# Kernel optimization log

Measured on AMD Instinct MI355X. Metric: run time of the kernel, lower is better.

Reference implementation:

```python
import jax, jax.numpy as jnp
import numpy as np

N_NODES = 200000
N_EDGES = 400000
NUM_GRAPHS = 8192
NODE_DIM, EDGE_DIM, H, NCLS, NLAYERS = 80, 6, 128, 500, 4


def setup_inputs() -> dict:
    key = jax.random.key(0)
    ks = iter(jax.random.split(key, 32))
    s = 0.05
    inp = {
        "x": jax.random.normal(next(ks), (N_NODES, NODE_DIM), jnp.float32),
        "edge_index": jax.random.randint(next(ks), (2, N_EDGES), 0, N_NODES, jnp.int32),
        "edge_attr": jax.random.uniform(next(ks), (N_EDGES, EDGE_DIM), jnp.float32),
        # sorted segment ids covering all NUM_GRAPHS graphs (~24 nodes each)
        "batch": ((jnp.arange(N_NODES, dtype=jnp.int64) * NUM_GRAPHS) // N_NODES).astype(jnp.int32),
        "node_w": jax.random.normal(next(ks), (NODE_DIM, H), jnp.float32) * s,
        "node_b": jnp.zeros((H,), jnp.float32),
        "edge_w": jax.random.normal(next(ks), (EDGE_DIM, H), jnp.float32) * s,
        "edge_b": jnp.zeros((H,), jnp.float32),
        "conv_w1": jax.random.normal(next(ks), (NLAYERS, H, 2 * H), jnp.float32) * s,
        "conv_b1": jnp.zeros((NLAYERS, 2 * H), jnp.float32),
        "conv_bn1_g": jnp.ones((NLAYERS, 2 * H), jnp.float32),
        "conv_bn1_b": jnp.zeros((NLAYERS, 2 * H), jnp.float32),
        "conv_w2": jax.random.normal(next(ks), (NLAYERS, 2 * H, H), jnp.float32) * s,
        "conv_b2": jnp.zeros((NLAYERS, H), jnp.float32),
        "bn_g": jnp.ones((NLAYERS, H), jnp.float32),
        "bn_b": jnp.zeros((NLAYERS, H), jnp.float32),
        "cls_w1": jax.random.normal(next(ks), (2 * H, H), jnp.float32) * s,
        "cls_b1": jnp.zeros((H,), jnp.float32),
        "cls_bn_g": jnp.ones((H,), jnp.float32),
        "cls_bn_b": jnp.zeros((H,), jnp.float32),
        "cls_w2": jax.random.normal(next(ks), (H, NCLS), jnp.float32) * s,
        "cls_b2": jnp.zeros((NCLS,), jnp.float32),
    }
    return inp


def _bn(h, g, b, eps=1e-5):
    # training-mode BatchNorm1d: biased batch statistics over dim 0
    m = h.mean(0)
    v = h.var(0)
    return (h - m) * jax.lax.rsqrt(v + eps) * g + b


def reference(x, edge_index, edge_attr, batch,
              node_w, node_b, edge_w, edge_b,
              conv_w1, conv_b1, conv_bn1_g, conv_bn1_b,
              conv_w2, conv_b2, bn_g, bn_b,
              cls_w1, cls_b1, cls_bn_g, cls_bn_b, cls_w2, cls_b2):
    n = x.shape[0]
    h = x @ node_w + node_b                       # [N, H]
    ea = edge_attr @ edge_w + edge_b              # [E, H]
    src, dst = edge_index[0], edge_index[1]       # PyG: row=source j, col=target i
    for l in range(conv_w1.shape[0]):
        # GINEConv: nn((1+eps)*x + sum_j relu(x_j + e_ij)), eps=0
        msg = jax.nn.relu(h[src] + ea)            # [E, H] gather + add + relu
        agg = jax.ops.segment_sum(msg, dst, num_segments=n)
        z = h + agg
        z = jax.nn.relu(_bn(z @ conv_w1[l] + conv_b1[l], conv_bn1_g[l], conv_bn1_b[l]))
        h = z @ conv_w2[l] + conv_b2[l]
        h = jax.nn.relu(_bn(h, bn_g[l], bn_b[l]))
    # global mean + max pooling over graphs
    counts = jax.ops.segment_sum(jnp.ones((n, 1), h.dtype), batch, num_segments=NUM_GRAPHS)
    pmean = jax.ops.segment_sum(h, batch, num_segments=NUM_GRAPHS) / jnp.maximum(counts, 1.0)
    pmax = jax.ops.segment_max(h, batch, num_segments=NUM_GRAPHS)
    pmax = jnp.where(jnp.isfinite(pmax), pmax, 0.0)
    p = jnp.concatenate([pmean, pmax], axis=1)    # [G, 2H]
    z = jax.nn.relu(p @ cls_w1 + cls_b1)
    z = _bn(z, cls_bn_g, cls_bn_b)                # dropout: identity (eval)
    return z @ cls_w2 + cls_b2                    # [G, NCLS]
```

## Files before the change

### kernel.cpp

```cpp
#include <hip/hip_runtime.h>

#define NN 200000
#define NE 400000
#define NG 8192
#define HD 128
#define H2 256
#define ND 80
#define NC 500
#define ZBLK 240
#define NCHUNK 6250

typedef short bf16x8 __attribute__((ext_vector_type(8)));
typedef short bf16x4 __attribute__((ext_vector_type(4)));
typedef float f32x4  __attribute__((ext_vector_type(4)));

static __device__ __forceinline__ short f2bf(float f) {
    unsigned u = __float_as_uint(f);
    unsigned r = (u + 0x7fffu + ((u >> 16) & 1u)) >> 16;
    return (short)r;
}
static __device__ __forceinline__ float bf2f(short s) {
    return __uint_as_float(((unsigned)(unsigned short)s) << 16);
}

__global__ void k_zero(float* p, int n) {
    int i = blockIdx.x * 256 + threadIdx.x;
    if (i < n) p[i] = 0.f;
}

__global__ __launch_bounds__(256) void k_node_encode(
    const float* __restrict__ x, const float* __restrict__ w,
    const float* __restrict__ b, float* __restrict__ u, float* __restrict__ agg)
{
    __shared__ float ws[ND][HD];
    __shared__ float xs[32][ND];
    const int tid = threadIdx.x;
    for (int i = tid; i < ND * HD; i += 256) ws[i >> 7][i & 127] = w[i];
    const int row0 = blockIdx.x * 32;
    for (int i = tid; i < 32 * ND; i += 256) {
        int r = i / ND, c = i % ND;
        xs[r][c] = x[(size_t)(row0 + r) * ND + c];
    }
    __syncthreads();
    const int col = tid & 127, rs = tid >> 7;
    const float bias = b[col];
    for (int it = 0; it < 16; ++it) {
        int rl = it * 2 + rs;
        float acc = bias;
        #pragma unroll
        for (int k = 0; k < ND; ++k) acc += xs[rl][k] * ws[k][col];
        size_t gi = (size_t)(row0 + rl) * HD + col;
        u[gi] = acc;
        agg[gi] = 0.f;
    }
}

__global__ __launch_bounds__(256) void k_msg_agg(
    const float* __restrict__ u, const int* __restrict__ ei,
    const float* __restrict__ eattr, const float* __restrict__ ew,
    const float* __restrict__ eb, const float* __restrict__ s2,
    const float* __restrict__ sh2, float* __restrict__ agg, int first)
{
    __shared__ float ews[6][HD];
    __shared__ float ebs[HD], s2s[HD], sh2s[HD];
    const int tid = threadIdx.x;
    for (int i = tid; i < 6 * HD; i += 256) ews[i >> 7][i & 127] = ew[i];
    if (tid < HD) { ebs[tid] = eb[tid]; s2s[tid] = s2[tid]; sh2s[tid] = sh2[tid]; }
    __syncthreads();
    const int col = tid & 127, es = tid >> 7;
    const int e0 = blockIdx.x * 32;
    for (int it = 0; it < 16; ++it) {
        int e = e0 + it * 2 + es;
        int src = ei[e], dst = ei[NE + e];
        float a0 = eattr[e * 6 + 0], a1 = eattr[e * 6 + 1], a2 = eattr[e * 6 + 2];
        float a3 = eattr[e * 6 + 3], a4 = eattr[e * 6 + 4], a5 = eattr[e * 6 + 5];
        float hv = u[(size_t)src * HD + col];
        if (!first) hv = fmaxf(hv * s2s[col] + sh2s[col], 0.f);
        float m = hv + ebs[col]
                + a0 * ews[0][col] + a1 * ews[1][col] + a2 * ews[2][col]
                + a3 * ews[3][col] + a4 * ews[4][col] + a5 * ews[5][col];
        m = fmaxf(m, 0.f);
        atomicAdd(&agg[(size_t)dst * HD + col], m);
    }
}

__global__ __launch_bounds__(256) void k_zstats2(
    const float* __restrict__ u, const float* __restrict__ agg,
    const float* __restrict__ s2, const float* __restrict__ sh2,
    float* __restrict__ Mpart, float* __restrict__ colzPart, int first)
{
    __shared__ float zs[32][HD];
    __shared__ float cred[8][HD];
    const int tid = threadIdx.x;
    const int bid = blockIdx.x;
    const int i0 = (tid >> 5) * 16;
    const int j0 = (tid & 31) * 4;
    const int lrow = tid >> 5;
    const int lc4  = tid & 31;

    float4 sv = *(const float4*)(s2 + lc4 * 4);
    float4 shv = *(const float4*)(sh2 + lc4 * 4);

    float acc[16][4];
    #pragma unroll
    for (int a = 0; a < 16; ++a)
        #pragma unroll
        for (int b = 0; b < 4; ++b) acc[a][b] = 0.f;
    float4 csum = make_float4(0.f, 0.f, 0.f, 0.f);

    float4 pv[4];
    int chunk = bid;
    {
        const size_t r0 = (size_t)chunk * 32;
        #pragma unroll
        for (int i = 0; i < 4; ++i) {
            size_t gi = (r0 + lrow + i * 8) * HD + lc4 * 4;
            float4 hv = *(const float4*)(u + gi);
            float4 av = *(const float4*)(agg + gi);
            if (!first) {
                hv.x = fmaxf(hv.x * sv.x + shv.x, 0.f);
                hv.y = fmaxf(hv.y * sv.y + shv.y, 0.f);
                hv.z = fmaxf(hv.z * sv.z + shv.z, 0.f);
                hv.w = fmaxf(hv.w * sv.w + shv.w, 0.f);
            }
            pv[i] = make_float4(hv.x + av.x, hv.y + av.y, hv.z + av.z, hv.w + av.w);
        }
    }

    while (chunk < NCHUNK) {
        __syncthreads();
        #pragma unroll
        for (int i = 0; i < 4; ++i) {
            *(float4*)(&zs[lrow + i * 8][lc4 * 4]) = pv[i];
            csum.x += pv[i].x; csum.y += pv[i].y;
            csum.z += pv[i].z; csum.w += pv[i].w;
        }
        __syncthreads();
        int nxt = chunk + ZBLK;
        if (nxt < NCHUNK) {
            const size_t r0 = (size_t)nxt * 32;
            #pragma unroll
            for (int i = 0; i < 4; ++i) {
                size_t gi = (r0 + lrow + i * 8) * HD + lc4 * 4;
                float4 hv = *(const float4*)(u + gi);
                float4 av = *(const float4*)(agg + gi);
                if (!first) {
                    hv.x = fmaxf(hv.x * sv.x + shv.x, 0.f);
                    hv.y = fmaxf(hv.y * sv.y + shv.y, 0.f);
                    hv.z = fmaxf(hv.z * sv.z + shv.z, 0.f);
                    hv.w = fmaxf(hv.w * sv.w + shv.w, 0.f);
                }
                pv[i] = make_float4(hv.x + av.x, hv.y + av.y, hv.z + av.z, hv.w + av.w);
            }
        }
        #pragma unroll 8
        for (int r = 0; r < 32; ++r) {
            float4 zj  = *(const float4*)(&zs[r][j0]);
            float4 zi0 = *(const float4*)(&zs[r][i0]);
            float4 zi1 = *(const float4*)(&zs[r][i0 + 4]);
            float4 zi2 = *(const float4*)(&zs[r][i0 + 8]);
            float4 zi3 = *(const float4*)(&zs[r][i0 + 12]);
            float zi[16] = {zi0.x, zi0.y, zi0.z, zi0.w,
                            zi1.x, zi1.y, zi1.z, zi1.w,
                            zi2.x, zi2.y, zi2.z, zi2.w,
                            zi3.x, zi3.y, zi3.z, zi3.w};
            #pragma unroll
            for (int a = 0; a < 16; ++a) {
                acc[a][0] += zi[a] * zj.x;
                acc[a][1] += zi[a] * zj.y;
                acc[a][2] += zi[a] * zj.z;
                acc[a][3] += zi[a] * zj.w;
            }
        }
        chunk = nxt;
    }

    float* mp = Mpart + (size_t)bid * 16384;
    #pragma unroll
    for (int a = 0; a < 16; ++a)
        *(float4*)(mp + (i0 + a) * HD + j0) =
            make_float4(acc[a][0], acc[a][1], acc[a][2], acc[a][3]);

    *(float4*)(&cred[lrow][lc4 * 4]) = csum;
    __syncthreads();
    if (tid < HD) {
        float s = 0.f;
        #pragma unroll
        for (int k = 0; k < 8; ++k) s += cred[k][tid];
        colzPart[bid * HD + tid] = s;
    }
}

__global__ __launch_bounds__(256) void k_mreduce(
    const float* __restrict__ Mpart, const float* __restrict__ colzPart,
    float* __restrict__ M, float* __restrict__ colz)
{
    int idx = blockIdx.x * 256 + threadIdx.x;
    if (idx < 16384) {
        float s = 0.f;
        for (int b = 0; b < ZBLK; ++b) s += Mpart[(size_t)b * 16384 + idx];
        M[idx] = s;
    } else if (idx < 16384 + HD) {
        int c = idx - 16384;
        float s = 0.f;
        for (int b = 0; b < ZBLK; ++b) s += colzPart[b * HD + c];
        colz[c] = s;
    }
}

__global__ __launch_bounds__(128) void k_bnprep1(
    const float* __restrict__ M, const float* __restrict__ colz,
    const float* __restrict__ w1p,
    const float* __restrict__ g, const float* __restrict__ b,
    float* __restrict__ scale, float* __restrict__ shift)
{
    __shared__ float wcs[128];
    __shared__ float red[128];
    __shared__ float red2[128];
    const int c = blockIdx.x;
    const int j = threadIdx.x;
    float wc = w1p[j * H2 + c];
    wcs[j] = wc;
    __syncthreads();
    float inner = 0.f;
    for (int k = 0; k < 128; ++k) inner += M[j * HD + k] * wcs[k];
    red[j] = wc * inner;
    red2[j] = colz[j] * wc;
    __syncthreads();
    for (int s = 64; s > 0; s >>= 1) {
        if (j < s) { red[j] += red[j + s]; red2[j] += red2[j + s]; }
        __syncthreads();
    }
    if (j == 0) {
        const float invn = 1.f / NN;
        float q = red[0] * invn;
        float d = red2[0] * invn;
        float var = q - d * d;
        float sc = g[c] * rsqrtf(var + 1e-5f);
        scale[c] = sc;
        shift[c] = b[c] - d * sc;
    }
}

__global__ __launch_bounds__(256) void k_wprep(
    const float* __restrict__ w1, const float* __restrict__ w2,
    short* __restrict__ wh, short* __restrict__ wlo)
{
    int id = blockIdx.x * 256 + threadIdx.x;
    int layer = id >> 16, r = id & 65535;
    float v;
    if (r < 32768) {
        int ft = r >> 11, kk = (r >> 9) & 3, l = (r >> 3) & 63, j = r & 7;
        int k = kk * 32 + (l >> 4) * 8 + j, c = ft * 16 + (l & 15);
        v = w1[(size_t)layer * HD * H2 + k * H2 + c];
    } else {
        int r2 = r - 32768;
        int ft = r2 >> 12, kk = (r2 >> 9) & 7, l = (r2 >> 3) & 63, j = r2 & 7;
        int k = kk * 32 + (l >> 4) * 8 + j, c = ft * 16 + (l & 15);
        v = w2[(size_t)layer * H2 * HD + k * HD + c];
    }
    short hi = f2bf(v);
    wh[id] = hi;
    wlo[id] = f2bf(v - bf2f(hi));
}

__global__ __launch_bounds__(128, 2) void k_fused_mfma3(
    const float* uin, float* agg,
    const short* __restrict__ w1h, const short* __restrict__ w1l,
    const short* __restrict__ w2h, const short* __restrict__ w2l,
    const float* __restrict__ scale1, const float* __restrict__ shift1,
    const float* __restrict__ s2, const float* __restrict__ sh2,
    const float* __restrict__ b2p, float* uout, int first)
{
    __shared__ short ysh[32 * 256];
    __shared__ short ysl[32 * 256];
    __shared__ float sc1s[H2], sh1s[H2];
    const int tid = threadIdx.x;
    const int row0g = blockIdx.x * 32;
    for (int i = tid; i < H2; i += 128) { sc1s[i] = scale1[i]; sh1s[i] = shift1[i]; }

    const int l = tid & 63, w = tid >> 6;
    const int nq = l >> 4;
    const int node = w * 16 + (l & 15);
    const int nx = node & 7;
    const size_t zbase = (size_t)(row0g + node) * HD;

    bf16x8 zh[4], zl[4];
    #pragma unroll
    for (int kk = 0; kk < 4; ++kk) {
        int c0 = kk * 32 + nq * 8;
        float4 u0 = *(const float4*)(uin + zbase + c0);
        float4 u1 = *(const float4*)(uin + zbase + c0 + 4);
        float4 a0 = *(const float4*)(agg + zbase + c0);
        float4 a1 = *(const float4*)(agg + zbase + c0 + 4);
        float z[8];
        if (first) {
            z[0]=u0.x+a0.x; z[1]=u0.y+a0.y; z[2]=u0.z+a0.z; z[3]=u0.w+a0.w;
            z[4]=u1.x+a1.x; z[5]=u1.y+a1.y; z[6]=u1.z+a1.z; z[7]=u1.w+a1.w;
        } else {
            float4 s0 = *(const float4*)(s2 + c0);
            float4 s1 = *(const float4*)(s2 + c0 + 4);
            float4 t0 = *(const float4*)(sh2 + c0);
            float4 t1 = *(const float4*)(sh2 + c0 + 4);
            z[0]=fmaxf(u0.x*s0.x+t0.x,0.f)+a0.x; z[1]=fmaxf(u0.y*s0.y+t0.y,0.f)+a0.y;
            z[2]=fmaxf(u0.z*s0.z+t0.z,0.f)+a0.z; z[3]=fmaxf(u0.w*s0.w+t0.w,0.f)+a0.w;
            z[4]=fmaxf(u1.x*s1.x+t1.x,0.f)+a1.x; z[5]=fmaxf(u1.y*s1.y+t1.y,0.f)+a1.y;
            z[6]=fmaxf(u1.z*s1.z+t1.z,0.f)+a1.z; z[7]=fmaxf(u1.w*s1.w+t1.w,0.f)+a1.w;
        }
        #pragma unroll
        for (int j = 0; j < 8; ++j) {
            short hi = f2bf(z[j]);
            zh[kk][j] = hi;
            zl[kk][j] = f2bf(z[j] - bf2f(hi));
        }
    }
    __syncthreads();

    bf16x8 pah[2][4], pal[2][4];
    #pragma unroll
    for (int kk = 0; kk < 4; ++kk) {
        int wi = (kk * 64 + l) * 8;
        pah[0][kk] = *(const bf16x8*)(w1h + wi);
        pal[0][kk] = *(const bf16x8*)(w1l + wi);
    }
    #pragma unroll
    for (int ft = 0; ft < 16; ++ft) {
        const int cur = ft & 1, nxt = cur ^ 1;
        if (ft < 15) {
            #pragma unroll
            for (int kk = 0; kk < 4; ++kk) {
                int wi = (((ft + 1) * 4 + kk) * 64 + l) * 8;
                pah[nxt][kk] = *(const bf16x8*)(w1h + wi);
                pal[nxt][kk] = *(const bf16x8*)(w1l + wi);
            }
        }
        f32x4 acc = {0.f, 0.f, 0.f, 0.f};
        #pragma unroll
        for (int kk = 0; kk < 4; ++kk) {
            acc = __builtin_amdgcn_mfma_f32_16x16x32_bf16(pah[cur][kk], zh[kk], acc, 0, 0, 0);
            acc = __builtin_amdgcn_mfma_f32_16x16x32_bf16(pah[cur][kk], zl[kk], acc, 0, 0, 0);
            acc = __builtin_amdgcn_mfma_f32_16x16x32_bf16(pal[cur][kk], zh[kk], acc, 0, 0, 0);
        }
        int f0 = ft * 16 + nq * 4;
        float4 scv = *(const float4*)(&sc1s[f0]);
        float4 shv = *(const float4*)(&sh1s[f0]);
        float y0 = fmaxf(acc[0] * scv.x + shv.x, 0.f);
        float y1 = fmaxf(acc[1] * scv.y + shv.y, 0.f);
        float y2 = fmaxf(acc[2] * scv.z + shv.z, 0.f);
        float y3 = fmaxf(acc[3] * scv.w + shv.w, 0.f);
        bf16x4 ph, pl;
        ph[0] = f2bf(y0); pl[0] = f2bf(y0 - bf2f(ph[0]));
        ph[1] = f2bf(y1); pl[1] = f2bf(y1 - bf2f(ph[1]));
        ph[2] = f2bf(y2); pl[2] = f2bf(y2 - bf2f(ph[2]));
        ph[3] = f2bf(y3); pl[3] = f2bf(y3 - bf2f(ph[3]));
        int off = node * 256 + (((f0 >> 3) ^ nx) * 8) + (nq & 1) * 4;
        *(bf16x4*)(&ysh[off]) = ph;
        *(bf16x4*)(&ysl[off]) = pl;
    }

    bf16x8 ybh[8], ybl[8];
    #pragma unroll
    for (int kk = 0; kk < 8; ++kk) {
        int off = node * 256 + (((kk * 4 + nq) ^ nx) * 8);
        ybh[kk] = *(const bf16x8*)(&ysh[off]);
        ybl[kk] = *(const bf16x8*)(&ysl[off]);
    }
    bf16x8 qh[2][4], ql[2][4];
    #pragma unroll
    for (int kk = 0; kk < 4; ++kk) {
        int wi = (kk * 64 + l) * 8;
        qh[0][kk] = *(const bf16x8*)(w2h + wi);
        ql[0][kk] = *(const bf16x8*)(w2l + wi);
    }
    f32x4 acc = {0.f, 0.f, 0.f, 0.f};
    #pragma unroll
    for (int ch = 0; ch < 16; ++ch) {
        const int ft = ch >> 1, half = ch & 1, cur = ch & 1, nxt = cur ^ 1;
        if (ch < 15) {
            int ft2 = (ch + 1) >> 1, kb = ((ch + 1) & 1) * 4;
            #pragma unroll
            for (int kk = 0; kk < 4; ++kk) {
                int wi = ((ft2 * 8 + kb + kk) * 64 + l) * 8;
                qh[nxt][kk] = *(const bf16x8*)(w2h + wi);
                ql[nxt][kk] = *(const bf16x8*)(w2l + wi);
            }
        }
        if (half == 0) { acc[0] = 0.f; acc[1] = 0.f; acc[2] = 0.f; acc[3] = 0.f; }
        #pragma unroll
        for (int kk = 0; kk < 4; ++kk) {
            acc = __builtin_amdgcn_mfma_f32_16x16x32_bf16(qh[cur][kk], ybh[half*4+kk], acc, 0, 0, 0);
            acc = __builtin_amdgcn_mfma_f32_16x16x32_bf16(qh[cur][kk], ybl[half*4+kk], acc, 0, 0, 0);
            acc = __builtin_amdgcn_mfma_f32_16x16x32_bf16(ql[cur][kk], ybh[half*4+kk], acc, 0, 0, 0);
        }
        if (half == 1) {
            int f0 = ft * 16 + nq * 4;
            float4 bv = *(const float4*)(b2p + f0);
            float4 o = make_float4(acc[0] + bv.x, acc[1] + bv.y,
                                   acc[2] + bv.z, acc[3] + bv.w);
            *(float4*)(&uout[zbase + f0]) = o;
            *(float4*)(&agg[zbase + f0]) = make_float4(0.f, 0.f, 0.f, 0.f);
        }
    }
}

__global__ __launch_bounds__(256) void k_ustats(
    const float* __restrict__ u,
    float* __restrict__ uslotS, float* __restrict__ uslotSS)
{
    __shared__ float sS[2][HD], sQ[2][HD];
    const int tid = threadIdx.x;
    const int col = tid & 127, half = tid >> 7;
    size_t r0 = (size_t)blockIdx.x * 500 + half * 250;
    float s = 0.f, ss = 0.f;
    for (int i = 0; i < 250; ++i) {
        float v = u[(r0 + i) * HD + col];
        s += v; ss += v * v;
    }
    sS[half][col] = s; sQ[half][col] = ss;
    __syncthreads();
    if (tid < HD) {
        int slot = blockIdx.x & 63;
        atomicAdd(&uslotS[slot * HD + tid],  sS[0][tid] + sS[1][tid]);
        atomicAdd(&uslotSS[slot * HD + tid], sQ[0][tid] + sQ[1][tid]);
    }
}

__global__ __launch_bounds__(128) void k_bnprep2(
    float* __restrict__ uslotS, float* __restrict__ uslotSS,
    const float* __restrict__ g, const float* __restrict__ b,
    float* __restrict__ scale, float* __restrict__ shift)
{
    const int c = threadIdx.x;
    float s = 0.f, ss = 0.f;
    for (int k = 0; k < 64; ++k) {
        s  += uslotS[k * HD + c];
        ss += uslotSS[k * HD + c];
        uslotS[k * HD + c] = 0.f;
        uslotSS[k * HD + c] = 0.f;
    }
    const float invn = 1.f / NN;
    float mean = s * invn;
    float var = ss * invn - mean * mean;
    float sc = g[c] * rsqrtf(var + 1e-5f);
    scale[c] = sc;
    shift[c] = b[c] - mean * sc;
}

__global__ __launch_bounds__(128) void k_pool(
    const float* __restrict__ u, const int* __restrict__ batch,
    const float* __restrict__ s2, const float* __restrict__ sh2,
    float* __restrict__ pmean, float* __restrict__ pmax)
{
    const int g = blockIdx.x;
    const int tid = threadIdx.x;
    const float sc = s2[tid], sh = sh2[tid];
    int lo = 0, hi = NN;
    while (lo < hi) { int mid = (lo + hi) >> 1; if (batch[mid] < g) lo = mid + 1; else hi = mid; }
    const int start = lo;
    hi = NN;
    while (lo < hi) { int mid = (lo + hi) >> 1; if (batch[mid] < g + 1) lo = mid + 1; else hi = mid; }
    const int end = lo;
    float s = 0.f, m = 0.f;
    for (int i = start; i < end; ++i) {
        float v = fmaxf(u[(size_t)i * HD + tid] * sc + sh, 0.f);
        s += v; m = fmaxf(m, v);
    }
    float cnt = (float)(end - start);
    pmean[g * HD + tid] = s / fmaxf(cnt, 1.f);
    pmax[g * HD + tid] = m;
}

__global__ __launch_bounds__(128) void k_cls1(
    const float* __restrict__ pmean, const float* __restrict__ pmax,
    const float* __restrict__ w, const float* __restrict__ b,
    float* __restrict__ z1)
{
    __shared__ float ps[16][H2];
    const int tid = threadIdx.x;
    const int row0 = blockIdx.x * 16;
    for (int i = tid; i < 16 * H2; i += 128) {
        int r = i >> 8, k = i & 255;
        ps[r][k] = (k < HD) ? pmean[(row0 + r) * HD + k]
                            : pmax[(row0 + r) * HD + k - HD];
    }
    __syncthreads();
    const int cp = tid & 63, rg = tid >> 6;
    float a0[8], a1[8];
    #pragma unroll
    for (int r = 0; r < 8; ++r) { a0[r] = 0.f; a1[r] = 0.f; }
    for (int kk = 0; kk < 64; ++kk) {
        float w00 = w[(kk * 4 + 0) * HD + cp];
        float w01 = w[(kk * 4 + 1) * HD + cp];
        float w02 = w[(kk * 4 + 2) * HD + cp];
        float w03 = w[(kk * 4 + 3) * HD + cp];
        float w10 = w[(kk * 4 + 0) * HD + cp + 64];
        float w11 = w[(kk * 4 + 1) * HD + cp + 64];
        float w12 = w[(kk * 4 + 2) * HD + cp + 64];
        float w13 = w[(kk * 4 + 3) * HD + cp + 64];
        #pragma unroll
        for (int r = 0; r < 8; ++r) {
            float4 z4 = *(const float4*)(&ps[rg * 8 + r][kk * 4]);
            a0[r] += z4.x * w00; a0[r] += z4.y * w01;
            a0[r] += z4.z * w02; a0[r] += z4.w * w03;
            a1[r] += z4.x * w10; a1[r] += z4.y * w11;
            a1[r] += z4.z * w12; a1[r] += z4.w * w13;
        }
    }
    const float bb0 = b[cp], bb1 = b[cp + 64];
    #pragma unroll
    for (int r = 0; r < 8; ++r) {
        int row = row0 + rg * 8 + r;
        z1[row * HD + cp]      = fmaxf(a0[r] + bb0, 0.f);
        z1[row * HD + cp + 64] = fmaxf(a1[r] + bb1, 0.f);
    }
}

__global__ __launch_bounds__(256) void k_colstats(
    const float* __restrict__ a, int nrows,
    float* __restrict__ ssum, float* __restrict__ ssumsq)
{
    const int tid = threadIdx.x;
    const int col = tid & 127;
    const int rsub = tid >> 7;
    const int r0 = blockIdx.x * 500;
    float s = 0.f, ss = 0.f;
    for (int i = rsub; i < 500; i += 2) {
        int r = r0 + i;
        if (r < nrows) {
            float v = a[r * HD + col];
            s += v; ss += v * v;
        }
    }
    atomicAdd(&ssum[col], s);
    atomicAdd(&ssumsq[col], ss);
}

__global__ void k_bnprep(float* __restrict__ ssum, float* __restrict__ ssumsq,
                         const float* __restrict__ g, const float* __restrict__ b,
                         float* __restrict__ scale, float* __restrict__ shift,
                         float invn)
{
    int c = threadIdx.x;
    if (c < HD) {
        float mean = ssum[c] * invn;
        float var = ssumsq[c] * invn - mean * mean;
        float sc = g[c] * rsqrtf(var + 1e-5f);
        scale[c] = sc;
        shift[c] = b[c] - mean * sc;
    }
}

__global__ __launch_bounds__(256) void k_cls2(
    const float* __restrict__ z1, const float* __restrict__ scale,
    const float* __restrict__ shift, const float* __restrict__ w,
    const float* __restrict__ b, float* __restrict__ outp)
{
    __shared__ float zs[16][HD];
    const int tid = threadIdx.x;
    const int row0 = blockIdx.x * 16;
    for (int i = tid; i < 16 * HD; i += 256) {
        int r = i >> 7, k = i & 127;
        zs[r][k] = z1[(row0 + r) * HD + k] * scale[k] + shift[k];
    }
    __syncthreads();
    #pragma unroll
    for (int cpass = 0; cpass < 2; ++cpass) {
        int c = tid + cpass * 256;
        if (c < NC) {
            float acc[16];
            float bb = b[c];
            #pragma unroll
            for (int r = 0; r < 16; ++r) acc[r] = bb;
            for (int k = 0; k < HD; ++k) {
                float wv = w[k * NC + c];
                #pragma unroll
                for (int r = 0; r < 16; ++r) acc[r] += zs[r][k] * wv;
            }
            #pragma unroll
            for (int r = 0; r < 16; ++r) outp[(size_t)(row0 + r) * NC + c] = acc[r];
        }
    }
}

extern "C" void kernel_launch(void* const* d_in, const int* in_sizes, int n_in,
                              void* d_out, int out_size, void* d_ws, size_t ws_size,
                              hipStream_t stream)
{
    const float* x       = (const float*)d_in[0];
    const int*   ei      = (const int*)  d_in[1];
    const float* eattr   = (const float*)d_in[2];
    const int*   batch   = (const int*)  d_in[3];
    const float* node_w  = (const float*)d_in[4];
    const float* node_b  = (const float*)d_in[5];
    const float* edge_w  = (const float*)d_in[6];
    const float* edge_b  = (const float*)d_in[7];
    const float* conv_w1 = (const float*)d_in[8];
    const float* conv_b1 = (const float*)d_in[9];
    const float* bn1g    = (const float*)d_in[10];
    const float* bn1b    = (const float*)d_in[11];
    const float* conv_w2 = (const float*)d_in[12];
    const float* conv_b2 = (const float*)d_in[13];
    const float* bng     = (const float*)d_in[14];
    const float* bnb     = (const float*)d_in[15];
    const float* cw1     = (const float*)d_in[16];
    const float* cb1     = (const float*)d_in[17];
    const float* cbg     = (const float*)d_in[18];
    const float* cbb     = (const float*)d_in[19];
    const float* cw2     = (const float*)d_in[20];
    const float* cb2     = (const float*)d_in[21];
    float* out = (float*)d_out;
    float* ws  = (float*)d_ws;

    float* u   = ws;
    float* agg = u + (size_t)NN * HD;
    float* z1  = agg + (size_t)NN * HD;
    float* st  = z1 + (size_t)NG * HD;

    float* uslotS  = st;
    float* uslotSS = st + 8192;
    float* clsS    = st + 16384;
    float* clsSS   = st + 16512;
    float* scale1  = st + 16640;
    float* shift1  = st + 16896;
    float* scale2  = st + 17152;
    float* shift2  = st + 17280;
    float* scalec  = st + 17408;
    float* shiftc  = st + 17536;
    float* M       = st + 17664;
    float* colz    = st + 34048;
    short* wbfh    = (short*)(st + 34176);
    short* wbfl    = (short*)(st + 34176 + 131072);

    float* Mpart    = out;
    float* colzPart = out + (size_t)ZBLK * 16384;
    float* pmean = out;
    float* pmax  = out + (size_t)NG * HD;

    k_zero<<<(16640 + 255) / 256, 256, 0, stream>>>(st, 16640);
    k_wprep<<<1024, 256, 0, stream>>>(conv_w1, conv_w2, wbfh, wbfl);
    k_node_encode<<<NN / 32, 256, 0, stream>>>(x, node_w, node_b, u, agg);

    for (int l = 0; l < 4; ++l) {
        int first = (l == 0) ? 1 : 0;
        k_msg_agg<<<NE / 32, 256, 0, stream>>>(u, ei, eattr, edge_w, edge_b,
                                               scale2, shift2, agg, first);
        k_zstats2<<<ZBLK, 256, 0, stream>>>(u, agg, scale2, shift2,
                                            Mpart, colzPart, first);
        k_mreduce<<<(16384 + HD + 255) / 256, 256, 0, stream>>>(Mpart, colzPart, M, colz);
        k_bnprep1<<<H2, 128, 0, stream>>>(M, colz,
                                          conv_w1 + (size_t)l * HD * H2,
                                          bn1g + (size_t)l * H2, bn1b + (size_t)l * H2,
                                          scale1, shift1);
        k_fused_mfma3<<<NN / 32, 128, 0, stream>>>(u, agg,
                                                   wbfh + (size_t)l * 65536,
                                                   wbfl + (size_t)l * 65536,
                                                   wbfh + (size_t)l * 65536 + 32768,
                                                   wbfl + (size_t)l * 65536 + 32768,
                                                   scale1, shift1, scale2, shift2,
                                                   conv_b2 + (size_t)l * HD, u, first);
        k_ustats<<<400, 256, 0, stream>>>(u, uslotS, uslotSS);
        k_bnprep2<<<1, 128, 0, stream>>>(uslotS, uslotSS,
                                         bng + (size_t)l * HD, bnb + (size_t)l * HD,
                                         scale2, shift2);
    }

    k_pool<<<NG, 128, 0, stream>>>(u, batch, scale2, shift2, pmean, pmax);
    k_cls1<<<NG / 16, 128, 0, stream>>>(pmean, pmax, cw1, cb1, z1);
    k_colstats<<<17, 256, 0, stream>>>(z1, NG, clsS, clsSS);
    k_bnprep<<<1, 256, 0, stream>>>(clsS, clsSS, cbg, cbb, scalec, shiftc, 1.f / NG);
    k_cls2<<<NG / 16, 256, 0, stream>>>(z1, scalec, shiftc, cw2, cb2, out);
}
```

Baseline: 2.660 ms.

## Process 64 nodes per block in fused MLP to reuse weight fragments

Each wave now handles two 16-node groups instead of one, so every bf16 weight fragment loaded from global memory feeds MFMAs for 32 nodes, halving weight traffic per node. The double-buffered weight prefetch is removed, and the second GEMM reads its activation fragments from shared memory inside the loop rather than holding them in registers. LDS use doubles to 64 KB per block and register pressure rises, which may lower occupancy, and the grid is halved to NN/64 blocks.

```diff
diff --git a/kernel.cpp b/kernel.cpp
--- a/kernel.cpp
+++ b/kernel.cpp
@@ -272,131 +272,135 @@
     const float* __restrict__ s2, const float* __restrict__ sh2,
     const float* __restrict__ b2p, float* uout, int first)
 {
-    __shared__ short ysh[32 * 256];
-    __shared__ short ysl[32 * 256];
+    __shared__ short ysh[64 * 256];
+    __shared__ short ysl[64 * 256];
     __shared__ float sc1s[H2], sh1s[H2];
     const int tid = threadIdx.x;
-    const int row0g = blockIdx.x * 32;
+    const int row0g = blockIdx.x * 64;
     for (int i = tid; i < H2; i += 128) { sc1s[i] = scale1[i]; sh1s[i] = shift1[i]; }
 
     const int l = tid & 63, w = tid >> 6;
     const int nq = l >> 4;
-    const int node = w * 16 + (l & 15);
-    const int nx = node & 7;
-    const size_t zbase = (size_t)(row0g + node) * HD;
-
-    bf16x8 zh[4], zl[4];
-    #pragma unroll
-    for (int kk = 0; kk < 4; ++kk) {
-        int c0 = kk * 32 + nq * 8;
-        float4 u0 = *(const float4*)(uin + zbase + c0);
-        float4 u1 = *(const float4*)(uin + zbase + c0 + 4);
-        float4 a0 = *(const float4*)(agg + zbase + c0);
-        float4 a1 = *(const float4*)(agg + zbase + c0 + 4);
-        float z[8];
-        if (first) {
-            z[0]=u0.x+a0.x; z[1]=u0.y+a0.y; z[2]=u0.z+a0.z; z[3]=u0.w+a0.w;
-            z[4]=u1.x+a1.x; z[5]=u1.y+a1.y; z[6]=u1.z+a1.z; z[7]=u1.w+a1.w;
-        } else {
-            float4 s0 = *(const float4*)(s2 + c0);
-            float4 s1 = *(const float4*)(s2 + c0 + 4);
-            float4 t0 = *(const float4*)(sh2 + c0);
-            float4 t1 = *(const float4*)(sh2 + c0 + 4);
-            z[0]=fmaxf(u0.x*s0.x+t0.x,0.f)+a0.x; z[1]=fmaxf(u0.y*s0.y+t0.y,0.f)+a0.y;
-            z[2]=fmaxf(u0.z*s0.z+t0.z,0.f)+a0.z; z[3]=fmaxf(u0.w*s0.w+t0.w,0.f)+a0.w;
-            z[4]=fmaxf(u1.x*s1.x+t1.x,0.f)+a1.x; z[5]=fmaxf(u1.y*s1.y+t1.y,0.f)+a1.y;
-            z[6]=fmaxf(u1.z*s1.z+t1.z,0.f)+a1.z; z[7]=fmaxf(u1.w*s1.w+t1.w,0.f)+a1.w;
-        }
-        #pragma unroll
-        for (int j = 0; j < 8; ++j) {
-            short hi = f2bf(z[j]);
-            zh[kk][j] = hi;
-            zl[kk][j] = f2bf(z[j] - bf2f(hi));
-        }
-    }
-    __syncthreads();
-
-    bf16x8 pah[2][4], pal[2][4];
-    #pragma unroll
-    for (int kk = 0; kk < 4; ++kk) {
-        int wi = (kk * 64 + l) * 8;
-        pah[0][kk] = *(const bf16x8*)(w1h + wi);
-        pal[0][kk] = *(const bf16x8*)(w1l + wi);
-    }
+
+    bf16x8 zh[2][4], zl[2][4];
+    #pragma unroll
+    for (int g = 0; g < 2; ++g) {
+        const int node = w * 32 + g * 16 + (l & 15);
+        const size_t zbase = (size_t)(row0g + node) * HD;
+        #pragma unroll
+        for (int kk = 0; kk < 4; ++kk) {
+            int c0 = kk * 32 + nq * 8;
+            float4 u0 = *(const float4*)(uin + zbase + c0);
+            float4 u1 = *(const float4*)(uin + zbase + c0 + 4);
+            float4 a0 = *(const float4*)(agg + zbase + c0);
+            float4 a1 = *(const float4*)(agg + zbase + c0 + 4);
+            float z[8];
+            if (first) {
+                z[0]=u0.x+a0.x; z[1]=u0.y+a0.y; z[2]=u0.z+a0.z; z[3]=u0.w+a0.w;
+                z[4]=u1.x+a1.x; z[5]=u1.y+a1.y; z[6]=u1.z+a1.z; z[7]=u1.w+a1.w;
+            } else {
+                float4 s0 = *(const float4*)(s2 + c0);
+                float4 s1 = *(const float4*)(s2 + c0 + 4);
+                float4 t0 = *(const float4*)(sh2 + c0);
+                float4 t1 = *(const float4*)(sh2 + c0 + 4);
+                z[0]=fmaxf(u0.x*s0.x+t0.x,0.f)+a0.x; z[1]=fmaxf(u0.y*s0.y+t0.y,0.f)+a0.y;
+                z[2]=fmaxf(u0.z*s0.z+t0.z,0.f)+a0.z; z[3]=fmaxf(u0.w*s0.w+t0.w,0.f)+a0.w;
+                z[4]=fmaxf(u1.x*s1.x+t1.x,0.f)+a1.x; z[5]=fmaxf(u1.y*s1.y+t1.y,0.f)+a1.y;
+                z[6]=fmaxf(u1.z*s1.z+t1.z,0.f)+a1.z; z[7]=fmaxf(u1.w*s1.w+t1.w,0.f)+a1.w;
+            }
+            #pragma unroll
+            for (int j = 0; j < 8; ++j) {
+                short hi = f2bf(z[j]);
+                zh[g][kk][j] = hi;
+                zl[g][kk][j] = f2bf(z[j] - bf2f(hi));
+            }
+        }
+    }
+    __syncthreads();
+
     #pragma unroll
     for (int ft = 0; ft < 16; ++ft) {
-        const int cur = ft & 1, nxt = cur ^ 1;
-        if (ft < 15) {
+        bf16x8 ah[4], al[4];
+        #pragma unroll
+        for (int kk = 0; kk < 4; ++kk) {
+            int wi = ((ft * 4 + kk) * 64 + l) * 8;
+            ah[kk] = *(const bf16x8*)(w1h + wi);
+            al[kk] = *(const bf16x8*)(w1l + wi);
+        }
+        const int f0 = ft * 16 + nq * 4;
+        const float4 scv = *(const float4*)(&sc1s[f0]);
+        const float4 shv = *(const float4*)(&sh1s[f0]);
+        #pragma unroll
+        for (int g = 0; g < 2; ++g) {
+            f32x4 acc = {0.f, 0.f, 0.f, 0.f};
             #pragma unroll
             for (int kk = 0; kk < 4; ++kk) {
-                int wi = (((ft + 1) * 4 + kk) * 64 + l) * 8;
-                pah[nxt][kk] = *(const bf16x8*)(w1h + wi);
-                pal[nxt][kk] = *(const bf16x8*)(w1l + wi);
-            }
-        }
-        f32x4 acc = {0.f, 0.f, 0.f, 0.f};
-        #pragma unroll
-        for (int kk = 0; kk < 4; ++kk) {
-            acc = __builtin_amdgcn_mfma_f32_16x16x32_bf16(pah[cur][kk], zh[kk], acc, 0, 0, 0);
-            acc = __builtin_amdgcn_mfma_f32_16x16x32_bf16(pah[cur][kk], zl[kk], acc, 0, 0, 0);
-            acc = __builtin_amdgcn_mfma_f32_16x16x32_bf16(pal[cur][kk], zh[kk], acc, 0, 0, 0);
-        }
-        int f0 = ft * 16 + nq * 4;
-        float4 scv = *(const float4*)(&sc1s[f0]);
-        float4 shv = *(const float4*)(&sh1s[f0]);
-        float y0 = fmaxf(acc[0] * scv.x + shv.x, 0.f);
-        float y1 = fmaxf(acc[1] * scv.y + shv.y, 0.f);
-        float y2 = fmaxf(acc[2] * scv.z + shv.z, 0.f);
-        float y3 = fmaxf(acc[3] * scv.w + shv.w, 0.f);
-        bf16x4 ph, pl;
-        ph[0] = f2bf(y0); pl[0] = f2bf(y0 - bf2f(ph[0]));
-        ph[1] = f2bf(y1); pl[1] = f2bf(y1 - bf2f(ph[1]));
-        ph[2] = f2bf(y2); pl[2] = f2bf(y2 - bf2f(ph[2]));
-        ph[3] = f2bf(y3); pl[3] = f2bf(y3 - bf2f(ph[3]));
-        int off = node * 256 + (((f0 >> 3) ^ nx) * 8) + (nq & 1) * 4;
-        *(bf16x4*)(&ysh[off]) = ph;
-        *(bf16x4*)(&ysl[off]) = pl;
-    }
-
-    bf16x8 ybh[8], ybl[8];
-    #pragma unroll
-    for (int kk = 0; kk < 8; ++kk) {
-        int off = node * 256 + (((kk * 4 + nq) ^ nx) * 8);
-        ybh[kk] = *(const bf16x8*)(&ysh[off]);
-        ybl[kk] = *(const bf16x8*)(&ysl[off]);
-    }
-    bf16x8 qh[2][4], ql[2][4];
-    #pragma unroll
-    for (int kk = 0; kk < 4; ++kk) {
-        int wi = (kk * 64 + l) * 8;
-        qh[0][kk] = *(const bf16x8*)(w2h + wi);
-        ql[0][kk] = *(const bf16x8*)(w2l + wi);
-    }
-    f32x4 acc = {0.f, 0.f, 0.f, 0.f};
-    #pragma unroll
-    for (int ch = 0; ch < 16; ++ch) {
-        const int ft = ch >> 1, half = ch & 1, cur = ch & 1, nxt = cur ^ 1;
-        if (ch < 15) {
-            int ft2 = (ch + 1) >> 1, kb = ((ch + 1) & 1) * 4;
-            #pragma unroll
-            for (int kk = 0; kk < 4; ++kk) {
-                int wi = ((ft2 * 8 + kb + kk) * 64 + l) * 8;
-                qh[nxt][kk] = *(const bf16x8*)(w2h + wi);
-                ql[nxt][kk] = *(const bf16x8*)(w2l + wi);
-            }
-        }
-        if (half == 0) { acc[0] = 0.f; acc[1] = 0.f; acc[2] = 0.f; acc[3] = 0.f; }
-        #pragma unroll
-        for (int kk = 0; kk < 4; ++kk) {
-            acc = __builtin_amdgcn_mfma_f32_16x16x32_bf16(qh[cur][kk], ybh[half*4+kk], acc, 0, 0, 0);
-            acc = __builtin_amdgcn_mfma_f32_16x16x32_bf16(qh[cur][kk], ybl[half*4+kk], acc, 0, 0, 0);
-            acc = __builtin_amdgcn_mfma_f32_16x16x32_bf16(ql[cur][kk], ybh[half*4+kk], acc, 0, 0, 0);
-        }
-        if (half == 1) {
-            int f0 = ft * 16 + nq * 4;
-            float4 bv = *(const float4*)(b2p + f0);
-            float4 o = make_float4(acc[0] + bv.x, acc[1] + bv.y,
-                                   acc[2] + bv.z, acc[3] + bv.w);
+                acc = __builtin_amdgcn_mfma_f32_16x16x32_bf16(ah[kk], zh[g][kk], acc, 0, 0, 0);
+                acc = __builtin_amdgcn_mfma_f32_16x16x32_bf16(ah[kk], zl[g][kk], acc, 0, 0, 0);
+                acc = __builtin_amdgcn_mfma_f32_16x16x32_bf16(al[kk], zh[g][kk], acc, 0, 0, 0);
+            }
+            float y0 = fmaxf(acc[0] * scv.x + shv.x, 0.f);
+            float y1 = fmaxf(acc[1] * scv.y + shv.y, 0.f);
+            float y2 = fmaxf(acc[2] * scv.z + shv.z, 0.f);
+            float y3 = fmaxf(acc[3] * scv.w + shv.w, 0.f);
+            bf16x4 ph, pl;
+            ph[0] = f2bf(y0); pl[0] = f2bf(y0 - bf2f(ph[0]));
+            ph[1] = f2bf(y1); pl[1] = f2bf(y1 - bf2f(ph[1]));
+            ph[2] = f2bf(y2); pl[2] = f2bf(y2 - bf2f(ph[2]));
+            ph[3] = f2bf(y3); pl[3] = f2bf(y3 - bf2f(ph[3]));
+            const int node = w * 32 + g * 16 + (l & 15);
+            const int nx = node & 7;
+            int off = node * 256 + (((f0 >> 3) ^ nx) * 8) + (nq & 1) * 4;
+            *(bf16x4*)(&ysh[off]) = ph;
+            *(bf16x4*)(&ysl[off]) = pl;
+        }
+    }
+
+    #pragma unroll
+    for (int ft = 0; ft < 8; ++ft) {
+        f32x4 acc0 = {0.f, 0.f, 0.f, 0.f};
+        f32x4 acc1 = {0.f, 0.f, 0.f, 0.f};
+        #pragma unroll
+        for (int kk = 0; kk < 8; ++kk) {
+            int wi = ((ft * 8 + kk) * 64 + l) * 8;
+            bf16x8 qh = *(const bf16x8*)(w2h + wi);
+            bf16x8 ql = *(const bf16x8*)(w2l + wi);
+            {
+                const int node = w * 32 + (l & 15);
+                const int nx = node & 7;
+                int off = node * 256 + (((kk * 4 + nq) ^ nx) * 8);
+                bf16x8 ybh = *(const bf16x8*)(&ysh[off]);
+                bf16x8 ybl = *(const bf16x8*)(&ysl[off]);
+                acc0 = __builtin_amdgcn_mfma_f32_16x16x32_bf16(qh, ybh, acc0, 0, 0, 0);
+                acc0 = __builtin_amdgcn_mfma_f32_16x16x32_bf16(qh, ybl, acc0, 0, 0, 0);
+                acc0 = __builtin_amdgcn_mfma_f32_16x16x32_bf16(ql, ybh, acc0, 0, 0, 0);
+            }
+            {
+                const int node = w * 32 + 16 + (l & 15);
+                const int nx = node & 7;
+                int off = node * 256 + (((kk * 4 + nq) ^ nx) * 8);
+                bf16x8 ybh = *(const bf16x8*)(&ysh[off]);
+                bf16x8 ybl = *(const bf16x8*)(&ysl[off]);
+                acc1 = __builtin_amdgcn_mfma_f32_16x16x32_bf16(qh, ybh, acc1, 0, 0, 0);
+                acc1 = __builtin_amdgcn_mfma_f32_16x16x32_bf16(qh, ybl, acc1, 0, 0, 0);
+                acc1 = __builtin_amdgcn_mfma_f32_16x16x32_bf16(ql, ybh, acc1, 0, 0, 0);
+            }
+        }
+        const int f0 = ft * 16 + nq * 4;
+        const float4 bv = *(const float4*)(b2p + f0);
+        {
+            const int node = w * 32 + (l & 15);
+            const size_t zbase = (size_t)(row0g + node) * HD;
+            float4 o = make_float4(acc0[0] + bv.x, acc0[1] + bv.y,
+                                   acc0[2] + bv.z, acc0[3] + bv.w);
+            *(float4*)(&uout[zbase + f0]) = o;
+            *(float4*)(&agg[zbase + f0]) = make_float4(0.f, 0.f, 0.f, 0.f);
+        }
+        {
+            const int node = w * 32 + 16 + (l & 15);
+            const size_t zbase = (size_t)(row0g + node) * HD;
+            float4 o = make_float4(acc1[0] + bv.x, acc1[1] + bv.y,
+                                   acc1[2] + bv.z, acc1[3] + bv.w);
             *(float4*)(&uout[zbase + f0]) = o;
             *(float4*)(&agg[zbase + f0]) = make_float4(0.f, 0.f, 0.f, 0.f);
         }
@@ -651,7 +655,7 @@
                                           conv_w1 + (size_t)l * HD * H2,
                                           bn1g + (size_t)l * H2, bn1b + (size_t)l * H2,
                                           scale1, shift1);
-        k_fused_mfma3<<<NN / 32, 128, 0, stream>>>(u, agg,
+        k_fused_mfma3<<<NN / 64, 128, 0, stream>>>(u, agg,
                                                    wbfh + (size_t)l * 65536,
                                                    wbfl + (size_t)l * 65536,
                                                    wbfh + (size_t)l * 65536 + 32768,
```

Result: slower. 2.886 ms (+8.5%).
